# Optimization experiments

Measured on AMD Instinct MI355X. Metric: run time of the kernel, lower is better.

The kernel has to match this reference:

```python
import jax, jax.numpy as jnp
import numpy as np

# Classifier3Stage core of Reg_3stage (giga_depth), defaults: close_far_separation=False, c3_line_div=1
BS, CIN, H, W = 1, 128, 112, 320
CL = (16, 16, 16)          # classes per stage
PAD = (0, 8, 8)
C12 = CL[0] * CL[1]        # 256
C123 = C12 * CL[2]         # 4096
C1D = [128, 32, 32, CL[0] + 2 * PAD[0]]   # per-line grouped conv dims: 128->32->32->16
C2D = [128, 32, 32, CL[1] + 2 * PAD[1]]   # CondMul stage2 dims: 128->32->32->32
C3D = [128, 32, 32, CL[2] + 2 * PAD[2]]   # CondMul stage3 dims (in=ch_latent[0][i], out=ch_latent[1][i+1])


def setup_inputs() -> dict:
    key = jax.random.key(0)

    def p(i, shape):
        return jax.random.normal(jax.random.fold_in(key, i), shape, jnp.float32) * 0.05

    d = {"x_in": jax.random.normal(jax.random.fold_in(key, 0), (BS, CIN, H, W), jnp.float32)}
    for i in range(3):  # c1: per-line (grouped) 1x1 convs -> [H, out, in] weights
        d[f"w1_{i}"] = p(10 + 2 * i, (H, C1D[i + 1], C1D[i]))
        d[f"b1_{i}"] = p(11 + 2 * i, (H, C1D[i + 1]))
    for i in range(3):  # c2: CondMul over H*classes0 conditions
        d[f"w2_{i}"] = p(20 + 2 * i, (H * CL[0], C2D[i], C2D[i + 1]))
        d[f"b2_{i}"] = p(21 + 2 * i, (H * CL[0], C2D[i + 1]))
    for i in range(3):  # c3: CondMul over H*classes12 conditions
        d[f"w3_{i}"] = p(30 + 2 * i, (H * C12, C3D[i], C3D[i + 1]))
        d[f"b3_{i}"] = p(31 + 2 * i, (H * C12, C3D[i + 1]))
    return d


def _lrelu(v):
    return jnp.where(v >= 0, v, 0.01 * v)


def _condmul(x, inds, w, b):
    # x: [N, Cin], inds: [N] int32, w: [K, Cin, Cout], b: [K, Cout]
    return jnp.einsum('ni,nio->no', x, w[inds]) + b[inds]


def reference(x_in, w1_0, b1_0, w1_1, b1_1, w1_2, b1_2,
              w2_0, b2_0, w2_1, b2_1, w2_2, b2_2,
              w3_0, b3_0, w3_1, b3_1, w3_2, b3_2):
    bs, C, h, w = x_in.shape
    x = jnp.transpose(x_in, (0, 2, 3, 1))              # [bs,H,W,C] (far segment = x_in, per-line layout)
    # stage 1: per-line 1x1 grouped convs
    t = x
    for (wt, bt, last) in [(w1_0, b1_0, False), (w1_1, b1_1, False), (w1_2, b1_2, True)]:
        t = jnp.einsum('bhwi,hoi->bhwo', t, wt) + bt[None, :, None, :]
        if not last:
            t = _lrelu(t)
    inds1 = jnp.argmax(t, axis=-1).astype(jnp.int32)   # [bs,H,W]
    off = jnp.arange(h, dtype=jnp.int32)[None, :, None]
    x_l = x.reshape(-1, C)                             # rows in (b,h,w) order
    i1l = (inds1 + CL[0] * off).reshape(-1)
    # stage 2: CondMul chain routed by line*class1 index
    y = _lrelu(_condmul(x_l, i1l, w2_0, b2_0))
    y = _lrelu(_condmul(y, i1l, w2_1, b2_1))
    y = _condmul(y, i1l, w2_2, b2_2)                   # [N, 32]
    inds2 = jnp.argmax(y, axis=1).astype(jnp.int32).reshape(bs, h, w)
    inds12 = inds1 * CL[1] + (inds2 - PAD[1])
    i12l = (jnp.clip(inds12, 0, C12 - 1) + C12 * off).reshape(-1)  # c3_line_div=1 -> scaled == unscaled
    # stage 3: CondMul chain routed by line*classes12 index (close segment = x_in)
    z = _lrelu(_condmul(x_l, i12l, w3_0, b3_0))
    z = _lrelu(_condmul(z, i12l, w3_1, b3_1))
    z = _condmul(z, i12l, w3_2, b3_2)                  # [N, 32]
    inds3 = jnp.argmax(z, axis=1).astype(jnp.int32).reshape(bs, h, w)
    inds123 = jnp.clip(inds12 * CL[2] + (inds3 - PAD[2]), 0, C123 - 1)
    return inds123.reshape(bs, 1, h, w)
```

## Files before the change

kernel.cpp:

```cpp
#include <hip/hip_runtime.h>

#define HH   112
#define WW   320
#define CIN_ 128
#define HW_  (HH * WW)
#define CHUNK 32

__device__ __forceinline__ float lrelu(float v) {
    return v >= 0.f ? v : 0.01f * v;
}

__global__ __launch_bounds__(512, 2)
void k1_stage1(const float* __restrict__ x_in,
               const float* __restrict__ w1_0, const float* __restrict__ b1_0,
               const float* __restrict__ w1_1, const float* __restrict__ b1_1,
               const float* __restrict__ w1_2, const float* __restrict__ b1_2,
               int* __restrict__ inds1_out, float* __restrict__ xT_out,
               int* __restrict__ qc2, int* __restrict__ qc3)
{
    __shared__ float w1s0[32][CIN_ + 1];
    __shared__ float w1s1[32][33];
    __shared__ float w1s2[16][33];
    __shared__ float b1s[80];
    __shared__ float xT[16][132];

    const int h   = blockIdx.x >> 2;
    const int q   = blockIdx.x & 3;
    const int tid = threadIdx.x;
    const int base = h * WW;

    if (blockIdx.x == 0 && tid == 0) { *qc2 = 0; *qc3 = 0; }

    for (int n = tid; n < 32 * CIN_; n += 512)
        w1s0[n >> 7][n & 127] = w1_0[h * (32 * CIN_) + n];
    for (int n = tid; n < 32 * 32; n += 512)
        w1s1[n >> 5][n & 31] = w1_1[h * 1024 + n];
    if (tid < 16 * 32)
        w1s2[tid >> 5][tid & 31] = w1_2[h * 512 + tid];
    if      (tid < 32) b1s[tid] = b1_0[h * 32 + tid];
    else if (tid < 64) b1s[tid] = b1_1[h * 32 + (tid - 32)];
    else if (tid < 80) b1s[tid] = b1_2[h * 16 + (tid - 64)];
    __syncthreads();

    const int wave = tid >> 6;
    const int lane = tid & 63;
    const int o    = lane & 31;
    const int half = lane >> 5;
    const int o16  = lane & 15;

    for (int t = 0; t < 5; ++t) {
        const int w0 = q * 80 + t * 16;
        for (int n = tid; n < 16 * CIN_; n += 512) {
            int ww = n & 15, c = n >> 4;
            xT[ww][c] = x_in[c * HW_ + base + w0 + ww];
        }
        __syncthreads();
        for (int n = tid; n < 16 * CIN_; n += 512) {
            int pix = n >> 7, c = n & 127;
            xT_out[(size_t)(base + w0 + pix) * CIN_ + c] = xT[pix][c];
        }
        const float* xA = &xT[wave][0];
        const float* xB = &xT[wave + 8][0];

        float aA = 0.f, aB = 0.f;
        #pragma unroll
        for (int i = 0; i < 64; i += 4) {
            const int ii = half * 64 + i;
            const float w0v = w1s0[o][ii];
            const float w1v = w1s0[o][ii + 1];
            const float w2v = w1s0[o][ii + 2];
            const float w3v = w1s0[o][ii + 3];
            const float4 a4 = *reinterpret_cast<const float4*>(&xA[ii]);
            const float4 b4 = *reinterpret_cast<const float4*>(&xB[ii]);
            aA += a4.x * w0v;  aB += b4.x * w0v;
            aA += a4.y * w1v;  aB += b4.y * w1v;
            aA += a4.z * w2v;  aB += b4.z * w2v;
            aA += a4.w * w3v;  aB += b4.w * w3v;
        }
        aA += __shfl_xor(aA, 32);
        aB += __shfl_xor(aB, 32);
        float yA = lrelu(aA + b1s[o]);
        float yB = lrelu(aB + b1s[o]);

        aA = 0.f; aB = 0.f;
        #pragma unroll
        for (int i = 0; i < 32; ++i) {
            const float wv = w1s1[o][i];
            aA += __shfl(yA, i) * wv;
            aB += __shfl(yB, i) * wv;
        }
        float y2A = lrelu(aA + b1s[32 + o]);
        float y2B = lrelu(aB + b1s[32 + o]);

        aA = 0.f; aB = 0.f;
        #pragma unroll
        for (int i = 0; i < 32; ++i) {
            const float wv = w1s2[o16][i];
            aA += __shfl(y2A, i) * wv;
            aB += __shfl(y2B, i) * wv;
        }
        const float t1A = aA + b1s[64 + o16];
        const float t1B = aB + b1s[64 + o16];

        float bvA = t1A, bvB = t1B;
        int   biA = o16, biB = o16;
        #pragma unroll
        for (int d = 1; d < 16; d <<= 1) {
            float ovA = __shfl_xor(bvA, d), ovB = __shfl_xor(bvB, d);
            int   oiA = __shfl_xor(biA, d), oiB = __shfl_xor(biB, d);
            if (ovA > bvA || (ovA == bvA && oiA < biA)) { bvA = ovA; biA = oiA; }
            if (ovB > bvB || (ovB == bvB && oiB < biB)) { bvB = ovB; biB = oiB; }
        }
        if (lane == 0) {
            inds1_out[base + w0 + wave]     = biA;
            inds1_out[base + w0 + wave + 8] = biB;
        }
        __syncthreads();
    }
}

template <int BINS>
__global__ void sorter(const int* __restrict__ inds_in, int clipmax,
                       int* __restrict__ sorted, int4* __restrict__ queue,
                       int* __restrict__ qcount)
{
    __shared__ int cnt[BINS];
    __shared__ int scan[BINS];
    __shared__ int rank[BINS];

    const int h = blockIdx.x, tid = threadIdx.x, base = h * WW;
    if (tid < BINS) { cnt[tid] = 0; rank[tid] = 0; }
    __syncthreads();

    int c = -1;
    if (tid < WW) {
        c = inds_in[base + tid];
        c = min(max(c, 0), clipmax);
        atomicAdd(&cnt[c], 1);
    }
    __syncthreads();
    if (tid < BINS) scan[tid] = cnt[tid];
    __syncthreads();
    for (int s = 1; s < BINS; s <<= 1) {
        int v = 0;
        if (tid >= s && tid < BINS) v = scan[tid - s];
        __syncthreads();
        if (tid < BINS) scan[tid] += v;
        __syncthreads();
    }
    if (tid < WW) {
        int pos = (scan[c] - cnt[c]) + atomicAdd(&rank[c], 1);
        sorted[base + pos] = base + tid;
    }
    if (tid < BINS && cnt[tid] > 0) {
        int offc = scan[tid] - cnt[tid];
        for (int s0 = 0; s0 < cnt[tid]; s0 += CHUNK) {
            int qi = atomicAdd(qcount, 1);
            queue[qi] = make_int4(h, tid, base + offc + s0,
                                  min(CHUNK, cnt[tid] - s0));
        }
    }
}

template <int STAGE>
__global__ __launch_bounds__(256, 4)
void qk_compute(const float* __restrict__ xT_in, const int* __restrict__ sorted,
                const int4* __restrict__ queue, const int* __restrict__ qcount,
                const float* __restrict__ W0, const float* __restrict__ Bb0,
                const float* __restrict__ W1, const float* __restrict__ Bb1,
                const float* __restrict__ W2, const float* __restrict__ Bb2,
                const int* __restrict__ inds12_in, int* __restrict__ result)
{
    __shared__ float ws0[CIN_ * 32];
    __shared__ float ws1[32 * 32];
    __shared__ float ws2[32 * 32];
    __shared__ float bs[96];
    __shared__ float xbuf[8][CIN_];

    const int tid  = threadIdx.x;
    const int wave = tid >> 6;
    const int lane = tid & 63;
    const int o    = lane & 31;
    const int half = lane >> 5;

    const int qn = *qcount;
    for (int qi = blockIdx.x; qi < qn; qi += gridDim.x) {
        const int4 it4   = queue[qi];
        const int  c     = it4.y;
        const int  start = it4.z;
        const int  n     = it4.w;
        const int  key   = (STAGE == 2) ? (it4.x * 16 + c) : (it4.x * 256 + c);

        __syncthreads();
        for (int i = tid; i < 1024; i += 256)
            ((float4*)ws0)[i] = ((const float4*)(W0 + (size_t)key * 4096))[i];
        if (tid < 256) {
            ((float4*)ws1)[tid] = ((const float4*)(W1 + (size_t)key * 1024))[tid];
            ((float4*)ws2)[tid] = ((const float4*)(W2 + (size_t)key * 1024))[tid];
        }
        if      (tid < 32) bs[tid] = Bb0[(size_t)key * 32 + tid];
        else if (tid < 64) bs[tid] = Bb1[(size_t)key * 32 + (tid - 32)];
        else if (tid < 96) bs[tid] = Bb2[(size_t)key * 32 + (tid - 64)];
        __syncthreads();

        const int sA = wave * 2, sB = wave * 2 + 1;
        for (int t0 = wave * 2; t0 < n; t0 += 8) {
            const bool vB  = (t0 + 1) < n;
            const int pixA = sorted[start + t0];
            const int pixB = vB ? sorted[start + t0 + 1] : pixA;
            xbuf[sA][lane]      = xT_in[(size_t)pixA * CIN_ + lane];
            xbuf[sA][64 + lane] = xT_in[(size_t)pixA * CIN_ + 64 + lane];
            xbuf[sB][lane]      = xT_in[(size_t)pixB * CIN_ + lane];
            xbuf[sB][64 + lane] = xT_in[(size_t)pixB * CIN_ + 64 + lane];
            asm volatile("s_waitcnt vmcnt(0) lgkmcnt(0)" ::: "memory");
            const float* xA = &xbuf[sA][0];
            const float* xB = &xbuf[sB][0];

            float aA = 0.f, aB = 0.f;
            #pragma unroll
            for (int i = 0; i < 64; i += 4) {
                const int ii = half * 64 + i;
                const float w0v = ws0[(ii + 0) * 32 + o];
                const float w1v = ws0[(ii + 1) * 32 + o];
                const float w2v = ws0[(ii + 2) * 32 + o];
                const float w3v = ws0[(ii + 3) * 32 + o];
                const float4 a4 = *reinterpret_cast<const float4*>(&xA[ii]);
                const float4 b4 = *reinterpret_cast<const float4*>(&xB[ii]);
                aA += a4.x * w0v;  aB += b4.x * w0v;
                aA += a4.y * w1v;  aB += b4.y * w1v;
                aA += a4.z * w2v;  aB += b4.z * w2v;
                aA += a4.w * w3v;  aB += b4.w * w3v;
            }
            aA += __shfl_xor(aA, 32);
            aB += __shfl_xor(aB, 32);
            float yA = lrelu(aA + bs[o]);
            float yB = lrelu(aB + bs[o]);

            aA = 0.f; aB = 0.f;
            #pragma unroll
            for (int i = 0; i < 32; ++i) {
                const float wv = ws1[i * 32 + o];
                aA += __shfl(yA, i) * wv;
                aB += __shfl(yB, i) * wv;
            }
            float y2A = lrelu(aA + bs[32 + o]);
            float y2B = lrelu(aB + bs[32 + o]);

            aA = 0.f; aB = 0.f;
            #pragma unroll
            for (int i = 0; i < 32; ++i) {
                const float wv = ws2[i * 32 + o];
                aA += __shfl(y2A, i) * wv;
                aB += __shfl(y2B, i) * wv;
            }
            const float y3A = aA + bs[64 + o];
            const float y3B = aB + bs[64 + o];

            float bvA = y3A, bvB = y3B;
            int   biA = o,   biB = o;
            #pragma unroll
            for (int d = 1; d < 32; d <<= 1) {
                float ovA = __shfl_xor(bvA, d), ovB = __shfl_xor(bvB, d);
                int   oiA = __shfl_xor(biA, d), oiB = __shfl_xor(biB, d);
                if (ovA > bvA || (ovA == bvA && oiA < biA)) { bvA = ovA; biA = oiA; }
                if (ovB > bvB || (ovB == bvB && oiB < biB)) { bvB = ovB; biB = oiB; }
            }
            if (lane == 0) {
                if (STAGE == 2) {
                    result[pixA] = c * 16 + biA - 8;
                    if (vB) result[pixB] = c * 16 + biB - 8;
                } else {
                    int vA12 = inds12_in[pixA];
                    result[pixA] = min(max(vA12 * 16 + biA - 8, 0), 4095);
                    if (vB) {
                        int vB12 = inds12_in[pixB];
                        result[pixB] = min(max(vB12 * 16 + biB - 8, 0), 4095);
                    }
                }
            }
        }
    }
}

__global__ __launch_bounds__(512, 4)
void reg3_fused(const float* __restrict__ x_in,
                const float* __restrict__ w1_0, const float* __restrict__ b1_0,
                const float* __restrict__ w1_1, const float* __restrict__ b1_1,
                const float* __restrict__ w1_2, const float* __restrict__ b1_2,
                const float* __restrict__ w2_0, const float* __restrict__ b2_0,
                const float* __restrict__ w2_1, const float* __restrict__ b2_1,
                const float* __restrict__ w2_2, const float* __restrict__ b2_2,
                const float* __restrict__ w3_0, const float* __restrict__ b3_0,
                const float* __restrict__ w3_1, const float* __restrict__ b3_1,
                const float* __restrict__ w3_2, const float* __restrict__ b3_2,
                int* __restrict__ out)
{
    __shared__ float xT[8][CIN_ + 1];
    __shared__ float w1s0[32][CIN_ + 1];
    __shared__ float w1s1[32][33];
    __shared__ float w1s2[16][33];
    __shared__ float b1s[80];

    const int h   = blockIdx.x / 40;
    const int w0  = (blockIdx.x % 40) * 8;
    const int tid = threadIdx.x;

    for (int n = tid; n < 8 * CIN_; n += 512) {
        int ww = n & 7, c = n >> 3;
        xT[ww][c] = x_in[c * HW_ + h * WW + w0 + ww];
    }
    for (int n = tid; n < 32 * CIN_; n += 512)
        w1s0[n >> 7][n & 127] = w1_0[h * (32 * CIN_) + n];
    for (int n = tid; n < 32 * 32; n += 512)
        w1s1[n >> 5][n & 31] = w1_1[h * 1024 + n];
    if (tid < 16 * 32)
        w1s2[tid >> 5][tid & 31] = w1_2[h * 512 + tid];
    if      (tid < 32) b1s[tid] = b1_0[h * 32 + tid];
    else if (tid < 64) b1s[tid] = b1_1[h * 32 + (tid - 32)];
    else if (tid < 80) b1s[tid] = b1_2[h * 16 + (tid - 64)];
    __syncthreads();

    const int wave = tid >> 6, lane = tid & 63;
    const int o = lane & 31, half = lane >> 5, o16 = lane & 15;
    const float* xr = &xT[wave][0];

    float acc = 0.f;
    #pragma unroll
    for (int i = 0; i < 64; ++i) { int ii = half * 64 + i; acc += xr[ii] * w1s0[o][ii]; }
    acc += __shfl_xor(acc, 32);
    float y = lrelu(acc + b1s[o]);
    acc = 0.f;
    #pragma unroll
    for (int i = 0; i < 32; ++i) acc += __shfl(y, i) * w1s1[o][i];
    float y2 = lrelu(acc + b1s[32 + o]);
    acc = 0.f;
    #pragma unroll
    for (int i = 0; i < 32; ++i) acc += __shfl(y2, i) * w1s2[o16][i];
    float t1 = acc + b1s[64 + o16];

    float bv = t1; int bi = o16;
    #pragma unroll
    for (int d = 1; d < 16; d <<= 1) {
        float ov = __shfl_xor(bv, d); int oi = __shfl_xor(bi, d);
        if (ov > bv || (ov == bv && oi < bi)) { bv = ov; bi = oi; }
    }
    const int inds1 = bi;
    const int idx1  = inds1 + 16 * h;

    const float* Wp = w2_0 + (size_t)idx1 * (CIN_ * 32);
    acc = 0.f;
    #pragma unroll
    for (int i = 0; i < 64; ++i) { int ii = half * 64 + i; acc += xr[ii] * Wp[ii * 32 + o]; }
    acc += __shfl_xor(acc, 32);
    y = lrelu(acc + b2_0[idx1 * 32 + o]);
    Wp = w2_1 + (size_t)idx1 * 1024;
    acc = 0.f;
    #pragma unroll
    for (int i = 0; i < 32; ++i) acc += __shfl(y, i) * Wp[i * 32 + o];
    y2 = lrelu(acc + b2_1[idx1 * 32 + o]);
    Wp = w2_2 + (size_t)idx1 * 1024;
    acc = 0.f;
    #pragma unroll
    for (int i = 0; i < 32; ++i) acc += __shfl(y2, i) * Wp[i * 32 + o];
    float y3 = acc + b2_2[idx1 * 32 + o];

    bv = y3; bi = o;
    #pragma unroll
    for (int d = 1; d < 32; d <<= 1) {
        float ov = __shfl_xor(bv, d); int oi = __shfl_xor(bi, d);
        if (ov > bv || (ov == bv && oi < bi)) { bv = ov; bi = oi; }
    }
    const int inds2  = bi;
    const int inds12 = inds1 * 16 + inds2 - 8;
    const int clip12 = min(max(inds12, 0), 255);
    const int idx12  = clip12 + 256 * h;

    Wp = w3_0 + (size_t)idx12 * (CIN_ * 32);
    acc = 0.f;
    #pragma unroll
    for (int i = 0; i < 64; ++i) { int ii = half * 64 + i; acc += xr[ii] * Wp[ii * 32 + o]; }
    acc += __shfl_xor(acc, 32);
    y = lrelu(acc + b3_0[idx12 * 32 + o]);
    Wp = w3_1 + (size_t)idx12 * 1024;
    acc = 0.f;
    #pragma unroll
    for (int i = 0; i < 32; ++i) acc += __shfl(y, i) * Wp[i * 32 + o];
    y2 = lrelu(acc + b3_1[idx12 * 32 + o]);
    Wp = w3_2 + (size_t)idx12 * 1024;
    acc = 0.f;
    #pragma unroll
    for (int i = 0; i < 32; ++i) acc += __shfl(y2, i) * Wp[i * 32 + o];
    y3 = acc + b3_2[idx12 * 32 + o];

    bv = y3; bi = o;
    #pragma unroll
    for (int d = 1; d < 32; d <<= 1) {
        float ov = __shfl_xor(bv, d); int oi = __shfl_xor(bi, d);
        if (ov > bv || (ov == bv && oi < bi)) { bv = ov; bi = oi; }
    }
    int inds123 = inds12 * 16 + bi - 8;
    inds123 = min(max(inds123, 0), 4095);
    if (lane == 0) out[h * WW + w0 + wave] = inds123;
}

extern "C" void kernel_launch(void* const* d_in, const int* in_sizes, int n_in,
                              void* d_out, int out_size, void* d_ws, size_t ws_size,
                              hipStream_t stream)
{
    const float* x_in = (const float*)d_in[0];
    const float* w1_0 = (const float*)d_in[1];
    const float* b1_0 = (const float*)d_in[2];
    const float* w1_1 = (const float*)d_in[3];
    const float* b1_1 = (const float*)d_in[4];
    const float* w1_2 = (const float*)d_in[5];
    const float* b1_2 = (const float*)d_in[6];
    const float* w2_0 = (const float*)d_in[7];
    const float* b2_0 = (const float*)d_in[8];
    const float* w2_1 = (const float*)d_in[9];
    const float* b2_1 = (const float*)d_in[10];
    const float* w2_2 = (const float*)d_in[11];
    const float* b2_2 = (const float*)d_in[12];
    const float* w3_0 = (const float*)d_in[13];
    const float* b3_0 = (const float*)d_in[14];
    const float* w3_1 = (const float*)d_in[15];
    const float* b3_1 = (const float*)d_in[16];
    const float* w3_2 = (const float*)d_in[17];
    const float* b3_2 = (const float*)d_in[18];
    int* out = (int*)d_out;

    char* ws = (char*)d_ws;
    int*   inds1_ws  = (int*)(ws + 0);
    int*   inds12_ws = (int*)(ws + 143360);
    int*   sorted2   = (int*)(ws + 286720);
    int*   sorted3   = (int*)(ws + 430080);
    int*   qc2       = (int*)(ws + 573440);
    int*   qc3       = (int*)(ws + 573444);
    int4*  queue2    = (int4*)(ws + 573456);
    int4*  queue3    = (int4*)(ws + 1146896);
    float* xT_ws     = (float*)(ws + 1720336);
    const size_t NEED = 1720336 + (size_t)HW_ * CIN_ * 4;

    if (ws_size >= NEED) {
        k1_stage1<<<HH * 4, 512, 0, stream>>>(
            x_in, w1_0, b1_0, w1_1, b1_1, w1_2, b1_2,
            inds1_ws, xT_ws, qc2, qc3);
        sorter<16><<<HH, 512, 0, stream>>>(inds1_ws, 15, sorted2, queue2, qc2);
        qk_compute<2><<<2048, 256, 0, stream>>>(
            xT_ws, sorted2, queue2, qc2,
            w2_0, b2_0, w2_1, b2_1, w2_2, b2_2, nullptr, inds12_ws);
        sorter<256><<<HH, 512, 0, stream>>>(inds12_ws, 255, sorted3, queue3, qc3);
        qk_compute<3><<<2048, 256, 0, stream>>>(
            xT_ws, sorted3, queue3, qc3,
            w3_0, b3_0, w3_1, b3_1, w3_2, b3_2, inds12_ws, out);
    } else {
        reg3_fused<<<HH * 40, 512, 0, stream>>>(
            x_in, w1_0, b1_0, w1_1, b1_1, w1_2, b1_2,
            w2_0, b2_0, w2_1, b2_1, w2_2, b2_2,
            w3_0, b3_0, w3_1, b3_1, w3_2, b3_2, out);
    }
}
```

Baseline: 222.4 us.

## Process four pixels per wave in CondMul queue kernel and prefetch features early

The queue-driven CondMul kernel now gives each wave four pixels per round instead of two, and caps each work item at two rounds of 16 pixels. It loads the first round's pixel features before fetching the per-condition weights, so the gathers overlap with the weight loads, and it prefetches the second round's features before computing the first. Layers two and three read activations from a small shared buffer as float4 instead of lane shuffles, which reuses each weight read across more pixels. In exchange it uses more registers and shared memory per block, and it relies on items holding at most 32 pixels.

```diff
diff --git a/kernel.cpp b/kernel.cpp
--- a/kernel.cpp
+++ b/kernel.cpp
@@ -175,7 +175,8 @@
     __shared__ float ws1[32 * 32];
     __shared__ float ws2[32 * 32];
     __shared__ float bs[96];
-    __shared__ float xbuf[8][CIN_];
+    __shared__ float xbuf[16][CIN_];
+    __shared__ float ys[4][4][32];
 
     const int tid  = threadIdx.x;
     const int wave = tid >> 6;
@@ -190,33 +191,31 @@
         const int  start = it4.z;
         const int  n     = it4.w;
         const int  key   = (STAGE == 2) ? (it4.x * 16 + c) : (it4.x * 256 + c);
+        const int  nr    = (n + 15) >> 4;
 
         __syncthreads();
+
+        int pix0[4]; float2 px0[4];
+        #pragma unroll
+        for (int k = 0; k < 4; ++k) {
+            const int t = wave * 4 + k;
+            pix0[k] = sorted[start + min(t, n - 1)];
+            px0[k]  = *reinterpret_cast<const float2*>(
+                          &xT_in[(size_t)pix0[k] * CIN_ + 2 * lane]);
+        }
+
         for (int i = tid; i < 1024; i += 256)
             ((float4*)ws0)[i] = ((const float4*)(W0 + (size_t)key * 4096))[i];
-        if (tid < 256) {
-            ((float4*)ws1)[tid] = ((const float4*)(W1 + (size_t)key * 1024))[tid];
-            ((float4*)ws2)[tid] = ((const float4*)(W2 + (size_t)key * 1024))[tid];
-        }
+        ((float4*)ws1)[tid] = ((const float4*)(W1 + (size_t)key * 1024))[tid];
+        ((float4*)ws2)[tid] = ((const float4*)(W2 + (size_t)key * 1024))[tid];
         if      (tid < 32) bs[tid] = Bb0[(size_t)key * 32 + tid];
         else if (tid < 64) bs[tid] = Bb1[(size_t)key * 32 + (tid - 32)];
         else if (tid < 96) bs[tid] = Bb2[(size_t)key * 32 + (tid - 64)];
         __syncthreads();
 
-        const int sA = wave * 2, sB = wave * 2 + 1;
-        for (int t0 = wave * 2; t0 < n; t0 += 8) {
-            const bool vB  = (t0 + 1) < n;
-            const int pixA = sorted[start + t0];
-            const int pixB = vB ? sorted[start + t0 + 1] : pixA;
-            xbuf[sA][lane]      = xT_in[(size_t)pixA * CIN_ + lane];
-            xbuf[sA][64 + lane] = xT_in[(size_t)pixA * CIN_ + 64 + lane];
-            xbuf[sB][lane]      = xT_in[(size_t)pixB * CIN_ + lane];
-            xbuf[sB][64 + lane] = xT_in[(size_t)pixB * CIN_ + 64 + lane];
-            asm volatile("s_waitcnt vmcnt(0) lgkmcnt(0)" ::: "memory");
-            const float* xA = &xbuf[sA][0];
-            const float* xB = &xbuf[sB][0];
-
-            float aA = 0.f, aB = 0.f;
+        auto compute_round = [&](int tb, const int* pixs) {
+            float acc[4] = {0.f, 0.f, 0.f, 0.f};
+
             #pragma unroll
             for (int i = 0; i < 64; i += 4) {
                 const int ii = half * 64 + i;
@@ -224,60 +223,115 @@
                 const float w1v = ws0[(ii + 1) * 32 + o];
                 const float w2v = ws0[(ii + 2) * 32 + o];
                 const float w3v = ws0[(ii + 3) * 32 + o];
-                const float4 a4 = *reinterpret_cast<const float4*>(&xA[ii]);
-                const float4 b4 = *reinterpret_cast<const float4*>(&xB[ii]);
-                aA += a4.x * w0v;  aB += b4.x * w0v;
-                aA += a4.y * w1v;  aB += b4.y * w1v;
-                aA += a4.z * w2v;  aB += b4.z * w2v;
-                aA += a4.w * w3v;  aB += b4.w * w3v;
-            }
-            aA += __shfl_xor(aA, 32);
-            aB += __shfl_xor(aB, 32);
-            float yA = lrelu(aA + bs[o]);
-            float yB = lrelu(aB + bs[o]);
-
-            aA = 0.f; aB = 0.f;
-            #pragma unroll
-            for (int i = 0; i < 32; ++i) {
-                const float wv = ws1[i * 32 + o];
-                aA += __shfl(yA, i) * wv;
-                aB += __shfl(yB, i) * wv;
-            }
-            float y2A = lrelu(aA + bs[32 + o]);
-            float y2B = lrelu(aB + bs[32 + o]);
-
-            aA = 0.f; aB = 0.f;
-            #pragma unroll
-            for (int i = 0; i < 32; ++i) {
-                const float wv = ws2[i * 32 + o];
-                aA += __shfl(y2A, i) * wv;
-                aB += __shfl(y2B, i) * wv;
-            }
-            const float y3A = aA + bs[64 + o];
-            const float y3B = aB + bs[64 + o];
-
-            float bvA = y3A, bvB = y3B;
-            int   biA = o,   biB = o;
+                #pragma unroll
+                for (int k = 0; k < 4; ++k) {
+                    const float4 a4 = *reinterpret_cast<const float4*>(
+                                          &xbuf[wave * 4 + k][ii]);
+                    acc[k] += a4.x * w0v;
+                    acc[k] += a4.y * w1v;
+                    acc[k] += a4.z * w2v;
+                    acc[k] += a4.w * w3v;
+                }
+            }
+            float y[4];
+            #pragma unroll
+            for (int k = 0; k < 4; ++k) {
+                acc[k] += __shfl_xor(acc[k], 32);
+                y[k] = lrelu(acc[k] + bs[o]);
+                ys[wave][k][o] = y[k];
+                acc[k] = 0.f;
+            }
+
+            #pragma unroll
+            for (int i = 0; i < 32; i += 4) {
+                const float w0v = ws1[(i + 0) * 32 + o];
+                const float w1v = ws1[(i + 1) * 32 + o];
+                const float w2v = ws1[(i + 2) * 32 + o];
+                const float w3v = ws1[(i + 3) * 32 + o];
+                #pragma unroll
+                for (int k = 0; k < 4; ++k) {
+                    const float4 y4 = *reinterpret_cast<const float4*>(&ys[wave][k][i]);
+                    acc[k] += y4.x * w0v;
+                    acc[k] += y4.y * w1v;
+                    acc[k] += y4.z * w2v;
+                    acc[k] += y4.w * w3v;
+                }
+            }
+            #pragma unroll
+            for (int k = 0; k < 4; ++k) {
+                const float y2 = lrelu(acc[k] + bs[32 + o]);
+                ys[wave][k][o] = y2;
+                acc[k] = 0.f;
+            }
+
+            #pragma unroll
+            for (int i = 0; i < 32; i += 4) {
+                const float w0v = ws2[(i + 0) * 32 + o];
+                const float w1v = ws2[(i + 1) * 32 + o];
+                const float w2v = ws2[(i + 2) * 32 + o];
+                const float w3v = ws2[(i + 3) * 32 + o];
+                #pragma unroll
+                for (int k = 0; k < 4; ++k) {
+                    const float4 y4 = *reinterpret_cast<const float4*>(&ys[wave][k][i]);
+                    acc[k] += y4.x * w0v;
+                    acc[k] += y4.y * w1v;
+                    acc[k] += y4.z * w2v;
+                    acc[k] += y4.w * w3v;
+                }
+            }
+            float y3[4];
+            #pragma unroll
+            for (int k = 0; k < 4; ++k) y3[k] = acc[k] + bs[64 + o];
+
+            float bv[4]; int bi[4];
+            #pragma unroll
+            for (int k = 0; k < 4; ++k) { bv[k] = y3[k]; bi[k] = o; }
             #pragma unroll
             for (int d = 1; d < 32; d <<= 1) {
-                float ovA = __shfl_xor(bvA, d), ovB = __shfl_xor(bvB, d);
-                int   oiA = __shfl_xor(biA, d), oiB = __shfl_xor(biB, d);
-                if (ovA > bvA || (ovA == bvA && oiA < biA)) { bvA = ovA; biA = oiA; }
-                if (ovB > bvB || (ovB == bvB && oiB < biB)) { bvB = ovB; biB = oiB; }
+                #pragma unroll
+                for (int k = 0; k < 4; ++k) {
+                    const float ov = __shfl_xor(bv[k], d);
+                    const int   oi = __shfl_xor(bi[k], d);
+                    if (ov > bv[k] || (ov == bv[k] && oi < bi[k])) { bv[k] = ov; bi[k] = oi; }
+                }
             }
             if (lane == 0) {
-                if (STAGE == 2) {
-                    result[pixA] = c * 16 + biA - 8;
-                    if (vB) result[pixB] = c * 16 + biB - 8;
-                } else {
-                    int vA12 = inds12_in[pixA];
-                    result[pixA] = min(max(vA12 * 16 + biA - 8, 0), 4095);
-                    if (vB) {
-                        int vB12 = inds12_in[pixB];
-                        result[pixB] = min(max(vB12 * 16 + biB - 8, 0), 4095);
+                #pragma unroll
+                for (int k = 0; k < 4; ++k) {
+                    const int t = tb + wave * 4 + k;
+                    if (t < n) {
+                        if (STAGE == 2) {
+                            result[pixs[k]] = c * 16 + bi[k] - 8;
+                        } else {
+                            const int v12 = inds12_in[pixs[k]];
+                            result[pixs[k]] = min(max(v12 * 16 + bi[k] - 8, 0), 4095);
+                        }
                     }
                 }
             }
+        };
+
+        #pragma unroll
+        for (int k = 0; k < 4; ++k)
+            *reinterpret_cast<float2*>(&xbuf[wave * 4 + k][2 * lane]) = px0[k];
+
+        int pix1[4]; float2 px1[4];
+        if (nr == 2) {
+            #pragma unroll
+            for (int k = 0; k < 4; ++k) {
+                const int t = 16 + wave * 4 + k;
+                pix1[k] = sorted[start + min(t, n - 1)];
+                px1[k]  = *reinterpret_cast<const float2*>(
+                              &xT_in[(size_t)pix1[k] * CIN_ + 2 * lane]);
+            }
+        }
+        compute_round(0, pix0);
+
+        if (nr == 2) {
+            #pragma unroll
+            for (int k = 0; k < 4; ++k)
+                *reinterpret_cast<float2*>(&xbuf[wave * 4 + k][2 * lane]) = px1[k];
+            compute_round(16, pix1);
         }
     }
 }
```

Result: slower. 705.2 us (+217.1%).

## Process four pixels per wave and prefetch pixel features before weight loads

Applied to the files above, without the earlier changes.

The CondMul queue kernel now handles four pixels per wave instead of two, so each LDS weight read is reused across four accumulators. It passes hidden activations through shared memory as float4 reads instead of 32 per-lane shuffles. Pixel feature loads for the first round are issued before the weight staging, and second-round loads are issued before the first round computes, so global latency overlaps with weight copies and compute. This relies on chunks holding at most 32 pixels (two rounds of 16) and raises register and LDS use per block.

```diff
diff --git a/kernel.cpp b/kernel.cpp
--- a/kernel.cpp
+++ b/kernel.cpp
@@ -162,6 +162,97 @@
     }
 }
 
+#define COMPUTE_ROUND(TB, PA, PB, PC, PD)                                      \
+{                                                                              \
+    float a0 = 0.f, a1 = 0.f, a2 = 0.f, a3 = 0.f;                              \
+    _Pragma("unroll")                                                          \
+    for (int i = 0; i < 64; i += 4) {                                          \
+        const int ii = half * 64 + i;                                          \
+        const float w0v = ws0[(ii + 0) * 32 + o];                              \
+        const float w1v = ws0[(ii + 1) * 32 + o];                              \
+        const float w2v = ws0[(ii + 2) * 32 + o];                              \
+        const float w3v = ws0[(ii + 3) * 32 + o];                              \
+        const float4 v0 = *reinterpret_cast<const float4*>(&xbuf[wave*4+0][ii]);\
+        const float4 v1 = *reinterpret_cast<const float4*>(&xbuf[wave*4+1][ii]);\
+        const float4 v2 = *reinterpret_cast<const float4*>(&xbuf[wave*4+2][ii]);\
+        const float4 v3 = *reinterpret_cast<const float4*>(&xbuf[wave*4+3][ii]);\
+        a0 += v0.x * w0v; a1 += v1.x * w0v; a2 += v2.x * w0v; a3 += v3.x * w0v;\
+        a0 += v0.y * w1v; a1 += v1.y * w1v; a2 += v2.y * w1v; a3 += v3.y * w1v;\
+        a0 += v0.z * w2v; a1 += v1.z * w2v; a2 += v2.z * w2v; a3 += v3.z * w2v;\
+        a0 += v0.w * w3v; a1 += v1.w * w3v; a2 += v2.w * w3v; a3 += v3.w * w3v;\
+    }                                                                          \
+    a0 += __shfl_xor(a0, 32); a1 += __shfl_xor(a1, 32);                        \
+    a2 += __shfl_xor(a2, 32); a3 += __shfl_xor(a3, 32);                        \
+    ys[wave][0][o] = lrelu(a0 + bs[o]);                                        \
+    ys[wave][1][o] = lrelu(a1 + bs[o]);                                        \
+    ys[wave][2][o] = lrelu(a2 + bs[o]);                                        \
+    ys[wave][3][o] = lrelu(a3 + bs[o]);                                        \
+    a0 = a1 = a2 = a3 = 0.f;                                                   \
+    _Pragma("unroll")                                                          \
+    for (int i = 0; i < 32; i += 4) {                                          \
+        const float w0v = ws1[(i + 0) * 32 + o];                               \
+        const float w1v = ws1[(i + 1) * 32 + o];                               \
+        const float w2v = ws1[(i + 2) * 32 + o];                               \
+        const float w3v = ws1[(i + 3) * 32 + o];                               \
+        const float4 y0 = *reinterpret_cast<const float4*>(&ys[wave][0][i]);   \
+        const float4 y1 = *reinterpret_cast<const float4*>(&ys[wave][1][i]);   \
+        const float4 y2 = *reinterpret_cast<const float4*>(&ys[wave][2][i]);   \
+        const float4 y3 = *reinterpret_cast<const float4*>(&ys[wave][3][i]);   \
+        a0 += y0.x * w0v; a1 += y1.x * w0v; a2 += y2.x * w0v; a3 += y3.x * w0v;\
+        a0 += y0.y * w1v; a1 += y1.y * w1v; a2 += y2.y * w1v; a3 += y3.y * w1v;\
+        a0 += y0.z * w2v; a1 += y1.z * w2v; a2 += y2.z * w2v; a3 += y3.z * w2v;\
+        a0 += y0.w * w3v; a1 += y1.w * w3v; a2 += y2.w * w3v; a3 += y3.w * w3v;\
+    }                                                                          \
+    ys[wave][0][o] = lrelu(a0 + bs[32 + o]);                                   \
+    ys[wave][1][o] = lrelu(a1 + bs[32 + o]);                                   \
+    ys[wave][2][o] = lrelu(a2 + bs[32 + o]);                                   \
+    ys[wave][3][o] = lrelu(a3 + bs[32 + o]);                                   \
+    a0 = a1 = a2 = a3 = 0.f;                                                   \
+    _Pragma("unroll")                                                          \
+    for (int i = 0; i < 32; i += 4) {                                          \
+        const float w0v = ws2[(i + 0) * 32 + o];                               \
+        const float w1v = ws2[(i + 1) * 32 + o];                               \
+        const float w2v = ws2[(i + 2) * 32 + o];                               \
+        const float w3v = ws2[(i + 3) * 32 + o];                               \
+        const float4 y0 = *reinterpret_cast<const float4*>(&ys[wave][0][i]);   \
+        const float4 y1 = *reinterpret_cast<const float4*>(&ys[wave][1][i]);   \
+        const float4 y2 = *reinterpret_cast<const float4*>(&ys[wave][2][i]);   \
+        const float4 y3 = *reinterpret_cast<const float4*>(&ys[wave][3][i]);   \
+        a0 += y0.x * w0v; a1 += y1.x * w0v; a2 += y2.x * w0v; a3 += y3.x * w0v;\
+        a0 += y0.y * w1v; a1 += y1.y * w1v; a2 += y2.y * w1v; a3 += y3.y * w1v;\
+        a0 += y0.z * w2v; a1 += y1.z * w2v; a2 += y2.z * w2v; a3 += y3.z * w2v;\
+        a0 += y0.w * w3v; a1 += y1.w * w3v; a2 += y2.w * w3v; a3 += y3.w * w3v;\
+    }                                                                          \
+    float bv0 = a0 + bs[64 + o], bv1 = a1 + bs[64 + o];                        \
+    float bv2 = a2 + bs[64 + o], bv3 = a3 + bs[64 + o];                        \
+    int bi0 = o, bi1 = o, bi2 = o, bi3 = o;                                    \
+    _Pragma("unroll")                                                          \
+    for (int d = 1; d < 32; d <<= 1) {                                         \
+        const float ov0 = __shfl_xor(bv0, d); const int oi0 = __shfl_xor(bi0, d);\
+        const float ov1 = __shfl_xor(bv1, d); const int oi1 = __shfl_xor(bi1, d);\
+        const float ov2 = __shfl_xor(bv2, d); const int oi2 = __shfl_xor(bi2, d);\
+        const float ov3 = __shfl_xor(bv3, d); const int oi3 = __shfl_xor(bi3, d);\
+        if (ov0 > bv0 || (ov0 == bv0 && oi0 < bi0)) { bv0 = ov0; bi0 = oi0; }  \
+        if (ov1 > bv1 || (ov1 == bv1 && oi1 < bi1)) { bv1 = ov1; bi1 = oi1; }  \
+        if (ov2 > bv2 || (ov2 == bv2 && oi2 < bi2)) { bv2 = ov2; bi2 = oi2; }  \
+        if (ov3 > bv3 || (ov3 == bv3 && oi3 < bi3)) { bv3 = ov3; bi3 = oi3; }  \
+    }                                                                          \
+    if (lane == 0) {                                                           \
+        const int tb4 = (TB) + wave * 4;                                       \
+        if (STAGE == 2) {                                                      \
+            if (tb4 + 0 < n) result[PA] = c * 16 + bi0 - 8;                    \
+            if (tb4 + 1 < n) result[PB] = c * 16 + bi1 - 8;                    \
+            if (tb4 + 2 < n) result[PC] = c * 16 + bi2 - 8;                    \
+            if (tb4 + 3 < n) result[PD] = c * 16 + bi3 - 8;                    \
+        } else {                                                               \
+            if (tb4 + 0 < n) result[PA] = min(max(inds12_in[PA] * 16 + bi0 - 8, 0), 4095); \
+            if (tb4 + 1 < n) result[PB] = min(max(inds12_in[PB] * 16 + bi1 - 8, 0), 4095); \
+            if (tb4 + 2 < n) result[PC] = min(max(inds12_in[PC] * 16 + bi2 - 8, 0), 4095); \
+            if (tb4 + 3 < n) result[PD] = min(max(inds12_in[PD] * 16 + bi3 - 8, 0), 4095); \
+        }                                                                      \
+    }                                                                          \
+}
+
 template <int STAGE>
 __global__ __launch_bounds__(256, 4)
 void qk_compute(const float* __restrict__ xT_in, const int* __restrict__ sorted,
@@ -175,7 +266,8 @@
     __shared__ float ws1[32 * 32];
     __shared__ float ws2[32 * 32];
     __shared__ float bs[96];
-    __shared__ float xbuf[8][CIN_];
+    __shared__ float xbuf[16][CIN_];
+    __shared__ float ys[4][4][32];
 
     const int tid  = threadIdx.x;
     const int wave = tid >> 6;
@@ -190,94 +282,55 @@
         const int  start = it4.z;
         const int  n     = it4.w;
         const int  key   = (STAGE == 2) ? (it4.x * 16 + c) : (it4.x * 256 + c);
+        const int  nr    = (n + 15) >> 4;
+        const int  t0    = wave * 4;
 
         __syncthreads();
+
+        const int pA0 = sorted[start + min(t0 + 0, n - 1)];
+        const int pB0 = sorted[start + min(t0 + 1, n - 1)];
+        const int pC0 = sorted[start + min(t0 + 2, n - 1)];
+        const int pD0 = sorted[start + min(t0 + 3, n - 1)];
+        const float2 xA0 = *reinterpret_cast<const float2*>(&xT_in[(size_t)pA0 * CIN_ + 2 * lane]);
+        const float2 xB0 = *reinterpret_cast<const float2*>(&xT_in[(size_t)pB0 * CIN_ + 2 * lane]);
+        const float2 xC0 = *reinterpret_cast<const float2*>(&xT_in[(size_t)pC0 * CIN_ + 2 * lane]);
+        const float2 xD0 = *reinterpret_cast<const float2*>(&xT_in[(size_t)pD0 * CIN_ + 2 * lane]);
+
         for (int i = tid; i < 1024; i += 256)
             ((float4*)ws0)[i] = ((const float4*)(W0 + (size_t)key * 4096))[i];
-        if (tid < 256) {
-            ((float4*)ws1)[tid] = ((const float4*)(W1 + (size_t)key * 1024))[tid];
-            ((float4*)ws2)[tid] = ((const float4*)(W2 + (size_t)key * 1024))[tid];
-        }
+        ((float4*)ws1)[tid] = ((const float4*)(W1 + (size_t)key * 1024))[tid];
+        ((float4*)ws2)[tid] = ((const float4*)(W2 + (size_t)key * 1024))[tid];
         if      (tid < 32) bs[tid] = Bb0[(size_t)key * 32 + tid];
         else if (tid < 64) bs[tid] = Bb1[(size_t)key * 32 + (tid - 32)];
         else if (tid < 96) bs[tid] = Bb2[(size_t)key * 32 + (tid - 64)];
         __syncthreads();
 
-        const int sA = wave * 2, sB = wave * 2 + 1;
-        for (int t0 = wave * 2; t0 < n; t0 += 8) {
-            const bool vB  = (t0 + 1) < n;
-            const int pixA = sorted[start + t0];
-            const int pixB = vB ? sorted[start + t0 + 1] : pixA;
-            xbuf[sA][lane]      = xT_in[(size_t)pixA * CIN_ + lane];
-            xbuf[sA][64 + lane] = xT_in[(size_t)pixA * CIN_ + 64 + lane];
-            xbuf[sB][lane]      = xT_in[(size_t)pixB * CIN_ + lane];
-            xbuf[sB][64 + lane] = xT_in[(size_t)pixB * CIN_ + 64 + lane];
-            asm volatile("s_waitcnt vmcnt(0) lgkmcnt(0)" ::: "memory");
-            const float* xA = &xbuf[sA][0];
-            const float* xB = &xbuf[sB][0];
-
-            float aA = 0.f, aB = 0.f;
-            #pragma unroll
-            for (int i = 0; i < 64; i += 4) {
-                const int ii = half * 64 + i;
-                const float w0v = ws0[(ii + 0) * 32 + o];
-                const float w1v = ws0[(ii + 1) * 32 + o];
-                const float w2v = ws0[(ii + 2) * 32 + o];
-                const float w3v = ws0[(ii + 3) * 32 + o];
-                const float4 a4 = *reinterpret_cast<const float4*>(&xA[ii]);
-                const float4 b4 = *reinterpret_cast<const float4*>(&xB[ii]);
-                aA += a4.x * w0v;  aB += b4.x * w0v;
-                aA += a4.y * w1v;  aB += b4.y * w1v;
-                aA += a4.z * w2v;  aB += b4.z * w2v;
-                aA += a4.w * w3v;  aB += b4.w * w3v;
-            }
-            aA += __shfl_xor(aA, 32);
-            aB += __shfl_xor(aB, 32);
-            float yA = lrelu(aA + bs[o]);
-            float yB = lrelu(aB + bs[o]);
-
-            aA = 0.f; aB = 0.f;
-            #pragma unroll
-            for (int i = 0; i < 32; ++i) {
-                const float wv = ws1[i * 32 + o];
-                aA += __shfl(yA, i) * wv;
-                aB += __shfl(yB, i) * wv;
-            }
-            float y2A = lrelu(aA + bs[32 + o]);
-            float y2B = lrelu(aB + bs[32 + o]);
-
-            aA = 0.f; aB = 0.f;
-            #pragma unroll
-            for (int i = 0; i < 32; ++i) {
-                const float wv = ws2[i * 32 + o];
-                aA += __shfl(y2A, i) * wv;
-                aB += __shfl(y2B, i) * wv;
-            }
-            const float y3A = aA + bs[64 + o];
-            const float y3B = aB + bs[64 + o];
-
-            float bvA = y3A, bvB = y3B;
-            int   biA = o,   biB = o;
-            #pragma unroll
-            for (int d = 1; d < 32; d <<= 1) {
-                float ovA = __shfl_xor(bvA, d), ovB = __shfl_xor(bvB, d);
-                int   oiA = __shfl_xor(biA, d), oiB = __shfl_xor(biB, d);
-                if (ovA > bvA || (ovA == bvA && oiA < biA)) { bvA = ovA; biA = oiA; }
-                if (ovB > bvB || (ovB == bvB && oiB < biB)) { bvB = ovB; biB = oiB; }
-            }
-            if (lane == 0) {
-                if (STAGE == 2) {
-                    result[pixA] = c * 16 + biA - 8;
-                    if (vB) result[pixB] = c * 16 + biB - 8;
-                } else {
-                    int vA12 = inds12_in[pixA];
-                    result[pixA] = min(max(vA12 * 16 + biA - 8, 0), 4095);
-                    if (vB) {
-                        int vB12 = inds12_in[pixB];
-                        result[pixB] = min(max(vB12 * 16 + biB - 8, 0), 4095);
-                    }
-                }
-            }
+        *reinterpret_cast<float2*>(&xbuf[wave * 4 + 0][2 * lane]) = xA0;
+        *reinterpret_cast<float2*>(&xbuf[wave * 4 + 1][2 * lane]) = xB0;
+        *reinterpret_cast<float2*>(&xbuf[wave * 4 + 2][2 * lane]) = xC0;
+        *reinterpret_cast<float2*>(&xbuf[wave * 4 + 3][2 * lane]) = xD0;
+
+        int pA1 = 0, pB1 = 0, pC1 = 0, pD1 = 0;
+        float2 xA1 = {0.f, 0.f}, xB1 = {0.f, 0.f}, xC1 = {0.f, 0.f}, xD1 = {0.f, 0.f};
+        if (nr == 2) {
+            pA1 = sorted[start + min(16 + t0 + 0, n - 1)];
+            pB1 = sorted[start + min(16 + t0 + 1, n - 1)];
+            pC1 = sorted[start + min(16 + t0 + 2, n - 1)];
+            pD1 = sorted[start + min(16 + t0 + 3, n - 1)];
+            xA1 = *reinterpret_cast<const float2*>(&xT_in[(size_t)pA1 * CIN_ + 2 * lane]);
+            xB1 = *reinterpret_cast<const float2*>(&xT_in[(size_t)pB1 * CIN_ + 2 * lane]);
+            xC1 = *reinterpret_cast<const float2*>(&xT_in[(size_t)pC1 * CIN_ + 2 * lane]);
+            xD1 = *reinterpret_cast<const float2*>(&xT_in[(size_t)pD1 * CIN_ + 2 * lane]);
+        }
+
+        COMPUTE_ROUND(0, pA0, pB0, pC0, pD0)
+
+        if (nr == 2) {
+            *reinterpret_cast<float2*>(&xbuf[wave * 4 + 0][2 * lane]) = xA1;
+            *reinterpret_cast<float2*>(&xbuf[wave * 4 + 1][2 * lane]) = xB1;
+            *reinterpret_cast<float2*>(&xbuf[wave * 4 + 2][2 * lane]) = xC1;
+            *reinterpret_cast<float2*>(&xbuf[wave * 4 + 3][2 * lane]) = xD1;
+            COMPUTE_ROUND(16, pA1, pB1, pC1, pD1)
         }
     }
 }
```

Result: faster. 200.0 us (-10.1%).
